# Performance work log

Measured on AMD Instinct MI355X. Metric: run time of the kernel, lower is better.

Reference implementation:

```python
import jax, jax.numpy as jnp
import numpy as np

B = 2; QD = 128; H = QD; W = QD; NQ = QD * QD
EMBED = 256; HEADS = 8; POINTS = 4; D = EMBED // HEADS; FFN = 512


def setup_inputs() -> dict:
    key = jax.random.key(0)
    ks = jax.random.split(key, 16)
    s = 0.02
    rn = lambda k, shp: jax.random.normal(k, shp, jnp.float32) * s
    return {
        'q': jax.random.normal(ks[0], (B, NQ, EMBED), jnp.float32),
        'W_off': rn(ks[1], (EMBED, HEADS * POINTS * 2)),
        'b_off': rn(ks[2], (HEADS * POINTS * 2,)),
        'W_attn': rn(ks[3], (EMBED, HEADS * POINTS)),
        'b_attn': rn(ks[4], (HEADS * POINTS,)),
        'W_val': rn(ks[5], (EMBED, EMBED)),
        'b_val': rn(ks[6], (EMBED,)),
        'W_out': rn(ks[7], (EMBED, EMBED)),
        'b_out': rn(ks[8], (EMBED,)),
        'W1': rn(ks[9], (EMBED, FFN)),
        'b1': rn(ks[10], (FFN,)),
        'W2': rn(ks[11], (FFN, EMBED)),
        'b2': rn(ks[12], (EMBED,)),
        'gamma': jnp.ones((EMBED,), jnp.float32),
        'beta': jnp.zeros((EMBED,), jnp.float32),
    }


def _layernorm(x, g, b):
    m = x.mean(-1, keepdims=True)
    v = ((x - m) ** 2).mean(-1, keepdims=True)
    return (x - m) * jax.lax.rsqrt(v + 1e-5) * g + b


def _msda(q, W_off, b_off, W_attn, b_attn, W_val, b_val, W_out, b_out):
    # value projection; value == query here. (B, NQ, EMBED)
    value = q @ W_val + b_val
    v = value.reshape(B, NQ, HEADS, D).transpose(0, 2, 1, 3)  # (B, heads, Nv, D)

    off = (q @ W_off + b_off).reshape(B, NQ, HEADS, POINTS, 2)
    aw = jax.nn.softmax((q @ W_attn + b_attn).reshape(B, NQ, HEADS, POINTS), axis=-1)

    # reference points: torch.meshgrid(linspace, linspace, indexing='xy')
    lin = jnp.linspace(0.0, 1.0, QD)
    gx, gy = jnp.meshgrid(lin, lin, indexing='xy')
    ref = jnp.stack([gx, gy], -1).reshape(1, NQ, 1, 1, 2)

    # offset_normalizer = [W, H]; sampling locations in [0,1]
    loc = ref + off / jnp.array([W, H], jnp.float32)
    # grid_sample bilinear, align_corners=False: pixel = loc * size - 0.5
    px = (loc[..., 0] * W - 0.5).transpose(0, 2, 1, 3)  # (B, heads, NQ, P)
    py = (loc[..., 1] * H - 0.5).transpose(0, 2, 1, 3)

    x0 = jnp.floor(px)
    y0 = jnp.floor(py)
    sampled = jnp.zeros((B, HEADS, NQ, POINTS, D), jnp.float32)
    for dy in (0.0, 1.0):
        for dx in (0.0, 1.0):
            xi = x0 + dx
            yi = y0 + dy
            wgt = (1.0 - jnp.abs(px - xi)) * (1.0 - jnp.abs(py - yi))
            valid = ((xi >= 0) & (xi <= W - 1) & (yi >= 0) & (yi <= H - 1)).astype(jnp.float32)
            idx = (jnp.clip(yi, 0, H - 1).astype(jnp.int32) * W
                   + jnp.clip(xi, 0, W - 1).astype(jnp.int32))  # (B, heads, NQ, P)
            g = jnp.take_along_axis(v, idx.reshape(B, HEADS, NQ * POINTS, 1), axis=2)
            g = g.reshape(B, HEADS, NQ, POINTS, D)
            sampled = sampled + g * (wgt * valid)[..., None]

    awt = aw.transpose(0, 2, 1, 3)  # (B, heads, NQ, P)
    out = (sampled * awt[..., None]).sum(3)  # (B, heads, NQ, D)
    out = out.transpose(0, 2, 1, 3).reshape(B, NQ, EMBED)
    # mmcv: dropout(output_proj(out)) + identity ; dropout is identity at eval
    return out @ W_out + b_out + q


def reference(q, W_off, b_off, W_attn, b_attn, W_val, b_val, W_out, b_out,
              W1, b1, W2, b2, gamma, beta):
    attn = _msda(q, W_off, b_off, W_attn, b_attn, W_val, b_val, W_out, b_out)
    x = attn + q  # outer residual in the module (in addition to mmcv's internal one)
    ffn = _layernorm(jax.nn.relu(x @ W1 + b1) @ W2 + b2, gamma, beta)
    return x + ffn
```

## Files before the change

kernel.cpp:

```cpp
#include <hip/hip_runtime.h>
#include <hip/hip_bf16.h>
#include <cstddef>
#include <cstdint>

#define B_      2
#define QD_     128
#define NQ_     (QD_ * QD_)
#define EMBED_  256
#define HEADS_  8
#define POINTS_ 4
#define FFN_    512
#define RTOT_   (B_ * NQ_)
#define NCATP_  384

using bf16x8 = __attribute__((ext_vector_type(8))) short;
using f32x4  = __attribute__((ext_vector_type(4))) float;

__device__ __forceinline__ short f2bf(float f) {
    unsigned u = __float_as_uint(f);
    u += 0x7FFFu + ((u >> 16) & 1u);
    return (short)(u >> 16);
}
__device__ __forceinline__ float bf2f(short s) {
    return __uint_as_float(((unsigned)(unsigned short)s) << 16);
}

#define WCAT_ELEMS  (NCATP_ * 256)
#define WOUT_ELEMS  (256 * 256)
#define W1_ELEMS    (512 * 256)
#define W2_ELEMS    (256 * 512)
#define PREP_TOTAL  (WCAT_ELEMS + WOUT_ELEMS + W1_ELEMS + W2_ELEMS)

__global__ __launch_bounds__(256) void prep_weights(
        const float* __restrict__ Wv, const float* __restrict__ Wo,
        const float* __restrict__ Wa, const float* __restrict__ bv,
        const float* __restrict__ bo, const float* __restrict__ ba,
        const float* __restrict__ W_out, const float* __restrict__ W1,
        const float* __restrict__ W2,
        short* __restrict__ WcatT, short* __restrict__ WoutT,
        short* __restrict__ W1T, short* __restrict__ W2T,
        float* __restrict__ bcat) {
    int idx = blockIdx.x * 256 + threadIdx.x;
    if (idx < WCAT_ELEMS) {
        int c = idx >> 8, k = idx & 255;
        float v = 0.f;
        if (c < 256)      v = Wv[k * 256 + c];
        else if (c < 320) v = Wo[k * 64 + (c - 256)];
        else if (c < 352) v = Wa[k * 32 + (c - 320)];
        WcatT[idx] = f2bf(v);
    } else if (idx < WCAT_ELEMS + WOUT_ELEMS) {
        int j = idx - WCAT_ELEMS; int c = j >> 8, k = j & 255;
        WoutT[j] = f2bf(W_out[k * 256 + c]);
    } else if (idx < WCAT_ELEMS + WOUT_ELEMS + W1_ELEMS) {
        int j = idx - (WCAT_ELEMS + WOUT_ELEMS); int c = j >> 8, k = j & 255;
        W1T[j] = f2bf(W1[k * 512 + c]);
    } else if (idx < PREP_TOTAL) {
        int j = idx - (WCAT_ELEMS + WOUT_ELEMS + W1_ELEMS); int c = j >> 9, k = j & 511;
        W2T[j] = f2bf(W2[k * 256 + c]);
    }
    if (idx < NCATP_) {
        float v = 0.f;
        if (idx < 256)      v = bv[idx];
        else if (idx < 320) v = bo[idx - 256];
        else if (idx < 352) v = ba[idx - 320];
        bcat[idx] = v;
    }
}

__global__ __launch_bounds__(256) void cvt_bf16(const float* __restrict__ in,
                                                short* __restrict__ out) {
    const size_t i = (size_t)blockIdx.x * 256 + threadIdx.x;
    const float4 f0 = *(const float4*)(in + i * 8);
    const float4 f1 = *(const float4*)(in + i * 8 + 4);
    bf16x8 v;
    v[0] = f2bf(f0.x); v[1] = f2bf(f0.y); v[2] = f2bf(f0.z); v[3] = f2bf(f0.w);
    v[4] = f2bf(f1.x); v[5] = f2bf(f1.y); v[6] = f2bf(f1.z); v[7] = f2bf(f1.w);
    *(bf16x8*)(out + i * 8) = v;
}

enum { EP_RELU_BF16 = 1, EP_ADD2Q_BF16 = 2, EP_SPLIT = 3 };

template <int EP>
__global__ __launch_bounds__(256) void gemm_mfma(
        const short* __restrict__ A,
        const short* __restrict__ Bt,
        const float* __restrict__ bias,
        const short* __restrict__ extra,
        float* __restrict__ Cf,
        short* __restrict__ Cb,
        int M, int N, int K) {
    __shared__ __align__(16) short As[128 * 64];
    __shared__ __align__(16) short Bs[128 * 64];

    const int t    = threadIdx.x;
    const int ln   = t & 63;
    const int w    = t >> 6;
    const int wr   = w >> 1;
    const int wc   = w & 1;
    const int lrow = ln & 15;
    const int lkg  = ln >> 4;

    const int gx   = gridDim.x;
    const int nwg  = gx * gridDim.y;
    const int flat = blockIdx.y * gx + blockIdx.x;
    const int q8   = nwg >> 3;
    const int swz  = (flat & 7) * q8 + (flat >> 3);
    const int row0 = (swz / gx) * 128;
    const int col0 = (swz % gx) * 128;

    f32x4 acc[4][4] = {};

    for (int k0 = 0; k0 < K; k0 += 64) {
        #pragma unroll
        for (int j = 0; j < 4; ++j) {
            const int c0 = (w * 4 + j) * 64;
            const int c  = c0 + ln;
            const int r  = c >> 3;
            const int s  = (c & 7) ^ (r & 7);
            const short* ga = A  + (size_t)(row0 + r) * K + (k0 + s * 8);
            const short* gb = Bt + (size_t)(col0 + r) * K + (k0 + s * 8);
            __builtin_amdgcn_global_load_lds(
                (const __attribute__((address_space(1))) void*)ga,
                (__attribute__((address_space(3))) void*)&As[c0 * 8], 16, 0, 0);
            __builtin_amdgcn_global_load_lds(
                (const __attribute__((address_space(1))) void*)gb,
                (__attribute__((address_space(3))) void*)&Bs[c0 * 8], 16, 0, 0);
        }
        __syncthreads();

        #pragma unroll
        for (int ks = 0; ks < 2; ++ks) {
            const int slot = ((ks * 4 + lkg) ^ (lrow & 7)) * 8;
            bf16x8 af[4], bfr[4];
            #pragma unroll
            for (int m = 0; m < 4; ++m)
                af[m] = *(const bf16x8*)&As[(wr * 64 + m * 16 + lrow) * 64 + slot];
            #pragma unroll
            for (int n = 0; n < 4; ++n)
                bfr[n] = *(const bf16x8*)&Bs[(wc * 64 + n * 16 + lrow) * 64 + slot];
            #pragma unroll
            for (int m = 0; m < 4; ++m)
                #pragma unroll
                for (int n = 0; n < 4; ++n)
                    acc[m][n] = __builtin_amdgcn_mfma_f32_16x16x32_bf16(
                        af[m], bfr[n], acc[m][n], 0, 0, 0);
        }
        __syncthreads();
    }

    const int orow = (ln >> 4) * 4;
    const int ocol = ln & 15;
    #pragma unroll
    for (int m = 0; m < 4; ++m) {
        #pragma unroll
        for (int n = 0; n < 4; ++n) {
            const int col = col0 + wc * 64 + n * 16 + ocol;
            const float bv = bias[col];
            #pragma unroll
            for (int rr = 0; rr < 4; ++rr) {
                const int row = row0 + wr * 64 + m * 16 + orow + rr;
                float v = acc[m][n][rr] + bv;
                if (EP == EP_SPLIT) {
                    if (col < 256) Cb[(size_t)row * 256 + col] = f2bf(v);
                    else           Cf[(size_t)row * 128 + (col - 256)] = v;
                } else if (EP == EP_RELU_BF16) {
                    Cb[(size_t)row * N + col] = f2bf(fmaxf(v, 0.f));
                } else if (EP == EP_ADD2Q_BF16) {
                    v += 2.f * bf2f(extra[(size_t)row * N + col]);
                    Cb[(size_t)row * N + col] = f2bf(v);
                }
            }
        }
    }
}

__global__ __launch_bounds__(256) void gemm_ln(
        const short* __restrict__ A,
        const short* __restrict__ Bt,
        const float* __restrict__ bias,
        const short* __restrict__ xres,
        const float* __restrict__ gamma, const float* __restrict__ beta,
        float* __restrict__ out, int M, int K) {
    __shared__ __align__(16) short As[64 * 64];
    __shared__ __align__(16) short Bs[256 * 64];
    __shared__ float red[64][4][2];

    const int t    = threadIdx.x;
    const int ln   = t & 63;
    const int w    = t >> 6;
    const int lrow = ln & 15;
    const int lkg  = ln >> 4;
    const int row0 = blockIdx.x * 64;

    f32x4 acc[4][4] = {};

    for (int k0 = 0; k0 < K; k0 += 64) {
        #pragma unroll
        for (int j = 0; j < 2; ++j) {
            const int c0 = (w * 2 + j) * 64;
            const int c  = c0 + ln;
            const int r  = c >> 3;
            const int s  = (c & 7) ^ (r & 7);
            const short* ga = A + (size_t)(row0 + r) * K + (k0 + s * 8);
            __builtin_amdgcn_global_load_lds(
                (const __attribute__((address_space(1))) void*)ga,
                (__attribute__((address_space(3))) void*)&As[c0 * 8], 16, 0, 0);
        }
        #pragma unroll
        for (int j = 0; j < 8; ++j) {
            const int c0 = (w * 8 + j) * 64;
            const int c  = c0 + ln;
            const int r  = c >> 3;
            const int s  = (c & 7) ^ (r & 7);
            const short* gb = Bt + (size_t)r * K + (k0 + s * 8);
            __builtin_amdgcn_global_load_lds(
                (const __attribute__((address_space(1))) void*)gb,
                (__attribute__((address_space(3))) void*)&Bs[c0 * 8], 16, 0, 0);
        }
        __syncthreads();

        #pragma unroll
        for (int ks = 0; ks < 2; ++ks) {
            const int slot = ((ks * 4 + lkg) ^ (lrow & 7)) * 8;
            bf16x8 af[4], bfr[4];
            #pragma unroll
            for (int m = 0; m < 4; ++m)
                af[m] = *(const bf16x8*)&As[(m * 16 + lrow) * 64 + slot];
            #pragma unroll
            for (int n = 0; n < 4; ++n)
                bfr[n] = *(const bf16x8*)&Bs[(w * 64 + n * 16 + lrow) * 64 + slot];
            #pragma unroll
            for (int m = 0; m < 4; ++m)
                #pragma unroll
                for (int n = 0; n < 4; ++n)
                    acc[m][n] = __builtin_amdgcn_mfma_f32_16x16x32_bf16(
                        af[m], bfr[n], acc[m][n], 0, 0, 0);
        }
        __syncthreads();
    }

    const int orow = (ln >> 4) * 4;
    const int ocol = ln & 15;

    #pragma unroll
    for (int n = 0; n < 4; ++n) {
        const float bv = bias[w * 64 + n * 16 + ocol];
        #pragma unroll
        for (int m = 0; m < 4; ++m)
            #pragma unroll
            for (int rr = 0; rr < 4; ++rr)
                acc[m][n][rr] += bv;
    }

    #pragma unroll
    for (int m = 0; m < 4; ++m) {
        #pragma unroll
        for (int rr = 0; rr < 4; ++rr) {
            float s = 0.f, sq = 0.f;
            #pragma unroll
            for (int n = 0; n < 4; ++n) {
                const float v = acc[m][n][rr];
                s += v; sq += v * v;
            }
            #pragma unroll
            for (int o = 1; o < 16; o <<= 1) {
                s  += __shfl_xor(s, o, 64);
                sq += __shfl_xor(sq, o, 64);
            }
            if (ocol == 0) {
                const int row = m * 16 + orow + rr;
                red[row][w][0] = s;
                red[row][w][1] = sq;
            }
        }
    }
    __syncthreads();

    #pragma unroll
    for (int m = 0; m < 4; ++m) {
        #pragma unroll
        for (int rr = 0; rr < 4; ++rr) {
            const int row = m * 16 + orow + rr;
            float S  = red[row][0][0] + red[row][1][0] + red[row][2][0] + red[row][3][0];
            float SQ = red[row][0][1] + red[row][1][1] + red[row][2][1] + red[row][3][1];
            const float mean = S * (1.0f / 256.0f);
            const float var  = SQ * (1.0f / 256.0f) - mean * mean;
            const float rs   = rsqrtf(var + 1e-5f);
            const size_t rbase = (size_t)(row0 + row) * 256;
            #pragma unroll
            for (int n = 0; n < 4; ++n) {
                const int col = w * 64 + n * 16 + ocol;
                const float o = bf2f(xres[rbase + col])
                              + (acc[m][n][rr] - mean) * rs * gamma[col] + beta[col];
                out[rbase + col] = o;
            }
        }
    }
}

__global__ __launch_bounds__(256) void msda_sample(
        const float* __restrict__ pm, const short* __restrict__ vcomp,
        short* __restrict__ msda) {
    __shared__ int   s_off[8][32][4];
    __shared__ float s_c[8][32][4];

    const int t  = threadIdx.x;
    const int r0 = blockIdx.x * 8;
    const int bq = r0 >> 14;

    {
        const int g = t >> 5, cmb = t & 31, h = cmb >> 2, p = cmb & 3;
        const int r = r0 + g;
        const int n = r & (NQ_ - 1);
        const int gi = n >> 7, gj = n & 127;
        const float* pr = pm + (size_t)r * 128;

        const float l0 = pr[64 + h * 4 + 0], l1 = pr[64 + h * 4 + 1];
        const float l2 = pr[64 + h * 4 + 2], l3 = pr[64 + h * 4 + 3];
        const float mx = fmaxf(fmaxf(l0, l1), fmaxf(l2, l3));
        const float sum = expf(l0 - mx) + expf(l1 - mx) + expf(l2 - mx) + expf(l3 - mx);
        const float lp = pr[64 + h * 4 + p];
        const float aw = expf(lp - mx) / sum;

        const float ox = pr[h * 8 + p * 2 + 0];
        const float oy = pr[h * 8 + p * 2 + 1];
        const float px = (gj * (1.0f / 127.0f) + ox * (1.0f / 128.0f)) * 128.0f - 0.5f;
        const float py = (gi * (1.0f / 127.0f) + oy * (1.0f / 128.0f)) * 128.0f - 0.5f;
        const float x0f = floorf(px), y0f = floorf(py);
        const int   x0 = (int)x0f, y0 = (int)y0f;
        const float fx = px - x0f, fy = py - y0f;
        const int x0c = min(max(x0, 0), 127), x1c = min(max(x0 + 1, 0), 127);
        const int y0c = min(max(y0, 0), 127), y1c = min(max(y0 + 1, 0), 127);
        const float vx0 = ((unsigned)x0 <= 127u) ? 1.f : 0.f;
        const float vx1 = ((unsigned)(x0 + 1) <= 127u) ? 1.f : 0.f;
        const float vy0 = ((unsigned)y0 <= 127u) ? 1.f : 0.f;
        const float vy1 = ((unsigned)(y0 + 1) <= 127u) ? 1.f : 0.f;

        s_off[g][cmb][0] = (y0c * 128 + x0c) * 512;
        s_off[g][cmb][1] = (y0c * 128 + x1c) * 512;
        s_off[g][cmb][2] = (y1c * 128 + x0c) * 512;
        s_off[g][cmb][3] = (y1c * 128 + x1c) * 512;
        s_c[g][cmb][0] = aw * (1.f - fx) * (1.f - fy) * vx0 * vy0;
        s_c[g][cmb][1] = aw * fx * (1.f - fy) * vx1 * vy0;
        s_c[g][cmb][2] = aw * (1.f - fx) * fy * vx0 * vy1;
        s_c[g][cmb][3] = aw * fx * fy * vx1 * vy1;
    }
    __syncthreads();

    const int half = t >> 7;
    const int h    = (t >> 4) & 7;
    const int dd   = t & 15;
    const char* vb = (const char*)vcomp + ((size_t)bq * NQ_ * 256 + h * 32 + dd * 2) * 2;

    #pragma unroll
    for (int it = 0; it < 4; ++it) {
        const int g = it * 2 + half;
        float a0 = 0.f, a1 = 0.f;
        #pragma unroll
        for (int p = 0; p < 4; ++p) {
            const int cmb = h * 4 + p;
            #pragma unroll
            for (int k = 0; k < 4; ++k) {
                const unsigned u = *(const unsigned*)(vb + s_off[g][cmb][k]);
                const float c = s_c[g][cmb][k];
                a0 += c * __uint_as_float(u << 16);
                a1 += c * __uint_as_float(u & 0xffff0000u);
            }
        }
        const int r = r0 + g;
        const unsigned o = (unsigned)(unsigned short)f2bf(a0)
                         | ((unsigned)(unsigned short)f2bf(a1) << 16);
        *(unsigned*)&msda[(size_t)r * 256 + h * 32 + dd * 2] = o;
    }
}

extern "C" void kernel_launch(void* const* d_in, const int* in_sizes, int n_in,
                              void* d_out, int out_size, void* d_ws, size_t ws_size,
                              hipStream_t stream) {
    const float* q      = (const float*)d_in[0];
    const float* b_out  = (const float*)d_in[8];
    const float* b1     = (const float*)d_in[10];
    const float* b2     = (const float*)d_in[12];
    const float* gamma  = (const float*)d_in[13];
    const float* beta   = (const float*)d_in[14];

    float* out = (float*)d_out;

    char* w = (char*)d_ws;
    float* pm    = (float*)w; w += (size_t)RTOT_ * 128 * 4;
    short* vcomp = (short*)w; w += (size_t)RTOT_ * 256 * 2;
    short* qbf   = (short*)w; w += (size_t)RTOT_ * EMBED_ * 2;
    short* msda  = (short*)w; w += (size_t)RTOT_ * EMBED_ * 2;
    short* xbf   = (short*)w; w += (size_t)RTOT_ * EMBED_ * 2;
    short* hid   = (short*)w; w += (size_t)RTOT_ * FFN_ * 2;
    short* WcatT = (short*)w; w += WCAT_ELEMS * 2;
    short* WoutT = (short*)w; w += WOUT_ELEMS * 2;
    short* W1T   = (short*)w; w += W1_ELEMS * 2;
    short* W2T   = (short*)w; w += W2_ELEMS * 2;
    float* bcat  = (float*)w; w += NCATP_ * 4;

    prep_weights<<<(PREP_TOTAL + 255) / 256, 256, 0, stream>>>(
        (const float*)d_in[5], (const float*)d_in[1], (const float*)d_in[3],
        (const float*)d_in[6], (const float*)d_in[2], (const float*)d_in[4],
        (const float*)d_in[7], (const float*)d_in[9], (const float*)d_in[11],
        WcatT, WoutT, W1T, W2T, bcat);

    cvt_bf16<<<(RTOT_ * EMBED_ / 8 + 255) / 256, 256, 0, stream>>>(q, qbf);

    gemm_mfma<EP_SPLIT><<<dim3(NCATP_ / 128, RTOT_ / 128), 256, 0, stream>>>(
        qbf, WcatT, bcat, nullptr, pm, vcomp, RTOT_, NCATP_, EMBED_);

    msda_sample<<<RTOT_ / 8, 256, 0, stream>>>(pm, vcomp, msda);

    gemm_mfma<EP_ADD2Q_BF16><<<dim3(EMBED_ / 128, RTOT_ / 128), 256, 0, stream>>>(
        msda, WoutT, b_out, qbf, nullptr, xbf, RTOT_, EMBED_, EMBED_);

    gemm_mfma<EP_RELU_BF16><<<dim3(FFN_ / 128, RTOT_ / 128), 256, 0, stream>>>(
        xbf, W1T, b1, nullptr, nullptr, hid, RTOT_, FFN_, EMBED_);

    gemm_ln<<<RTOT_ / 64, 256, 0, stream>>>(
        hid, W2T, b2, xbf, gamma, beta, out, RTOT_, FFN_);
}
```

Before: 107.5 us.

## Double-buffer GEMM LDS tiles, widen LN GEMM tile, merge prep kernels

Both GEMM kernels now double-buffer their LDS tiles, so the async global-to-LDS loads for the next K step are issued before the current step's MFMA work. The fused GEMM+LayerNorm kernel moves to 128-row tiles with 512 threads (8 waves), which halves how often each block reloads the full W2 tile. The q-to-bf16 conversion is merged into the weight-prep kernel to save one launch. The cost is doubled LDS use per block, which lowers occupancy, most of all for gemm_ln at about 96KB. The loop also keeps a barrier at the end of every iteration.

```diff
diff --git a/kernel.cpp b/kernel.cpp
--- a/kernel.cpp
+++ b/kernel.cpp
@@ -30,8 +30,11 @@
 #define W1_ELEMS    (512 * 256)
 #define W2_ELEMS    (256 * 512)
 #define PREP_TOTAL  (WCAT_ELEMS + WOUT_ELEMS + W1_ELEMS + W2_ELEMS)
-
-__global__ __launch_bounds__(256) void prep_weights(
+#define CVT_BLOCKS  (RTOT_ * EMBED_ / 8 / 256)
+#define PREP_BLOCKS ((PREP_TOTAL + 255) / 256)
+
+__global__ __launch_bounds__(256) void prep_all(
+        const float* __restrict__ q, short* __restrict__ qbf,
         const float* __restrict__ Wv, const float* __restrict__ Wo,
         const float* __restrict__ Wa, const float* __restrict__ bv,
         const float* __restrict__ bo, const float* __restrict__ ba,
@@ -40,7 +43,18 @@
         short* __restrict__ WcatT, short* __restrict__ WoutT,
         short* __restrict__ W1T, short* __restrict__ W2T,
         float* __restrict__ bcat) {
-    int idx = blockIdx.x * 256 + threadIdx.x;
+    const int b = blockIdx.x;
+    if (b < CVT_BLOCKS) {
+        const size_t i = (size_t)b * 256 + threadIdx.x;
+        const float4 f0 = *(const float4*)(q + i * 8);
+        const float4 f1 = *(const float4*)(q + i * 8 + 4);
+        bf16x8 v;
+        v[0] = f2bf(f0.x); v[1] = f2bf(f0.y); v[2] = f2bf(f0.z); v[3] = f2bf(f0.w);
+        v[4] = f2bf(f1.x); v[5] = f2bf(f1.y); v[6] = f2bf(f1.z); v[7] = f2bf(f1.w);
+        *(bf16x8*)(qbf + i * 8) = v;
+        return;
+    }
+    int idx = (b - CVT_BLOCKS) * 256 + threadIdx.x;
     if (idx < WCAT_ELEMS) {
         int c = idx >> 8, k = idx & 255;
         float v = 0.f;
@@ -67,17 +81,6 @@
     }
 }
 
-__global__ __launch_bounds__(256) void cvt_bf16(const float* __restrict__ in,
-                                                short* __restrict__ out) {
-    const size_t i = (size_t)blockIdx.x * 256 + threadIdx.x;
-    const float4 f0 = *(const float4*)(in + i * 8);
-    const float4 f1 = *(const float4*)(in + i * 8 + 4);
-    bf16x8 v;
-    v[0] = f2bf(f0.x); v[1] = f2bf(f0.y); v[2] = f2bf(f0.z); v[3] = f2bf(f0.w);
-    v[4] = f2bf(f1.x); v[5] = f2bf(f1.y); v[6] = f2bf(f1.z); v[7] = f2bf(f1.w);
-    *(bf16x8*)(out + i * 8) = v;
-}
-
 enum { EP_RELU_BF16 = 1, EP_ADD2Q_BF16 = 2, EP_SPLIT = 3 };
 
 template <int EP>
@@ -89,8 +92,8 @@
         float* __restrict__ Cf,
         short* __restrict__ Cb,
         int M, int N, int K) {
-    __shared__ __align__(16) short As[128 * 64];
-    __shared__ __align__(16) short Bs[128 * 64];
+    __shared__ __align__(16) short As[2][128 * 64];
+    __shared__ __align__(16) short Bs[2][128 * 64];
 
     const int t    = threadIdx.x;
     const int ln   = t & 63;
@@ -110,7 +113,7 @@
 
     f32x4 acc[4][4] = {};
 
-    for (int k0 = 0; k0 < K; k0 += 64) {
+    auto stage = [&](int buf, int k0) {
         #pragma unroll
         for (int j = 0; j < 4; ++j) {
             const int c0 = (w * 4 + j) * 64;
@@ -121,23 +124,28 @@
             const short* gb = Bt + (size_t)(col0 + r) * K + (k0 + s * 8);
             __builtin_amdgcn_global_load_lds(
                 (const __attribute__((address_space(1))) void*)ga,
-                (__attribute__((address_space(3))) void*)&As[c0 * 8], 16, 0, 0);
+                (__attribute__((address_space(3))) void*)&As[buf][c0 * 8], 16, 0, 0);
             __builtin_amdgcn_global_load_lds(
                 (const __attribute__((address_space(1))) void*)gb,
-                (__attribute__((address_space(3))) void*)&Bs[c0 * 8], 16, 0, 0);
-        }
-        __syncthreads();
-
+                (__attribute__((address_space(3))) void*)&Bs[buf][c0 * 8], 16, 0, 0);
+        }
+    };
+
+    stage(0, 0);
+    __syncthreads();
+    int cur = 0;
+    for (int k0 = 0; k0 < K; k0 += 64) {
+        if (k0 + 64 < K) stage(cur ^ 1, k0 + 64);
         #pragma unroll
         for (int ks = 0; ks < 2; ++ks) {
             const int slot = ((ks * 4 + lkg) ^ (lrow & 7)) * 8;
             bf16x8 af[4], bfr[4];
             #pragma unroll
             for (int m = 0; m < 4; ++m)
-                af[m] = *(const bf16x8*)&As[(wr * 64 + m * 16 + lrow) * 64 + slot];
+                af[m] = *(const bf16x8*)&As[cur][(wr * 64 + m * 16 + lrow) * 64 + slot];
             #pragma unroll
             for (int n = 0; n < 4; ++n)
-                bfr[n] = *(const bf16x8*)&Bs[(wc * 64 + n * 16 + lrow) * 64 + slot];
+                bfr[n] = *(const bf16x8*)&Bs[cur][(wc * 64 + n * 16 + lrow) * 64 + slot];
             #pragma unroll
             for (int m = 0; m < 4; ++m)
                 #pragma unroll
@@ -146,6 +154,7 @@
                         af[m], bfr[n], acc[m][n], 0, 0, 0);
         }
         __syncthreads();
+        cur ^= 1;
     }
 
     const int orow = (ln >> 4) * 4;
@@ -174,27 +183,29 @@
     }
 }
 
-__global__ __launch_bounds__(256) void gemm_ln(
+__global__ __launch_bounds__(512) void gemm_ln(
         const short* __restrict__ A,
         const short* __restrict__ Bt,
         const float* __restrict__ bias,
         const short* __restrict__ xres,
         const float* __restrict__ gamma, const float* __restrict__ beta,
         float* __restrict__ out, int M, int K) {
-    __shared__ __align__(16) short As[64 * 64];
-    __shared__ __align__(16) short Bs[256 * 64];
-    __shared__ float red[64][4][2];
+    __shared__ __align__(16) short As[2][128 * 64];
+    __shared__ __align__(16) short Bs[2][256 * 64];
+    __shared__ float red[128][4][2];
 
     const int t    = threadIdx.x;
     const int ln   = t & 63;
     const int w    = t >> 6;
+    const int wr   = w >> 2;
+    const int wc   = w & 3;
     const int lrow = ln & 15;
     const int lkg  = ln >> 4;
-    const int row0 = blockIdx.x * 64;
+    const int row0 = blockIdx.x * 128;
 
     f32x4 acc[4][4] = {};
 
-    for (int k0 = 0; k0 < K; k0 += 64) {
+    auto stage = [&](int buf, int k0) {
         #pragma unroll
         for (int j = 0; j < 2; ++j) {
             const int c0 = (w * 2 + j) * 64;
@@ -204,31 +215,36 @@
             const short* ga = A + (size_t)(row0 + r) * K + (k0 + s * 8);
             __builtin_amdgcn_global_load_lds(
                 (const __attribute__((address_space(1))) void*)ga,
-                (__attribute__((address_space(3))) void*)&As[c0 * 8], 16, 0, 0);
-        }
-        #pragma unroll
-        for (int j = 0; j < 8; ++j) {
-            const int c0 = (w * 8 + j) * 64;
+                (__attribute__((address_space(3))) void*)&As[buf][c0 * 8], 16, 0, 0);
+        }
+        #pragma unroll
+        for (int j = 0; j < 4; ++j) {
+            const int c0 = (w * 4 + j) * 64;
             const int c  = c0 + ln;
             const int r  = c >> 3;
             const int s  = (c & 7) ^ (r & 7);
             const short* gb = Bt + (size_t)r * K + (k0 + s * 8);
             __builtin_amdgcn_global_load_lds(
                 (const __attribute__((address_space(1))) void*)gb,
-                (__attribute__((address_space(3))) void*)&Bs[c0 * 8], 16, 0, 0);
-        }
-        __syncthreads();
-
+                (__attribute__((address_space(3))) void*)&Bs[buf][c0 * 8], 16, 0, 0);
+        }
+    };
+
+    stage(0, 0);
+    __syncthreads();
+    int cur = 0;
+    for (int k0 = 0; k0 < K; k0 += 64) {
+        if (k0 + 64 < K) stage(cur ^ 1, k0 + 64);
         #pragma unroll
         for (int ks = 0; ks < 2; ++ks) {
             const int slot = ((ks * 4 + lkg) ^ (lrow & 7)) * 8;
             bf16x8 af[4], bfr[4];
             #pragma unroll
             for (int m = 0; m < 4; ++m)
-                af[m] = *(const bf16x8*)&As[(m * 16 + lrow) * 64 + slot];
+                af[m] = *(const bf16x8*)&As[cur][(wr * 64 + m * 16 + lrow) * 64 + slot];
             #pragma unroll
             for (int n = 0; n < 4; ++n)
-                bfr[n] = *(const bf16x8*)&Bs[(w * 64 + n * 16 + lrow) * 64 + slot];
+                bfr[n] = *(const bf16x8*)&Bs[cur][(wc * 64 + n * 16 + lrow) * 64 + slot];
             #pragma unroll
             for (int m = 0; m < 4; ++m)
                 #pragma unroll
@@ -237,6 +253,7 @@
                         af[m], bfr[n], acc[m][n], 0, 0, 0);
         }
         __syncthreads();
+        cur ^= 1;
     }
 
     const int orow = (ln >> 4) * 4;
@@ -244,7 +261,7 @@
 
     #pragma unroll
     for (int n = 0; n < 4; ++n) {
-        const float bv = bias[w * 64 + n * 16 + ocol];
+        const float bv = bias[wc * 64 + n * 16 + ocol];
         #pragma unroll
         for (int m = 0; m < 4; ++m)
             #pragma unroll
@@ -268,9 +285,9 @@
                 sq += __shfl_xor(sq, o, 64);
             }
             if (ocol == 0) {
-                const int row = m * 16 + orow + rr;
-                red[row][w][0] = s;
-                red[row][w][1] = sq;
+                const int row = wr * 64 + m * 16 + orow + rr;
+                red[row][wc][0] = s;
+                red[row][wc][1] = sq;
             }
         }
     }
@@ -280,19 +297,18 @@
     for (int m = 0; m < 4; ++m) {
         #pragma unroll
         for (int rr = 0; rr < 4; ++rr) {
-            const int row = m * 16 + orow + rr;
-            float S  = red[row][0][0] + red[row][1][0] + red[row][2][0] + red[row][3][0];
-            float SQ = red[row][0][1] + red[row][1][1] + red[row][2][1] + red[row][3][1];
+            const int row = wr * 64 + m * 16 + orow + rr;
+            const float S  = red[row][0][0] + red[row][1][0] + red[row][2][0] + red[row][3][0];
+            const float SQ = red[row][0][1] + red[row][1][1] + red[row][2][1] + red[row][3][1];
             const float mean = S * (1.0f / 256.0f);
             const float var  = SQ * (1.0f / 256.0f) - mean * mean;
             const float rs   = rsqrtf(var + 1e-5f);
             const size_t rbase = (size_t)(row0 + row) * 256;
             #pragma unroll
             for (int n = 0; n < 4; ++n) {
-                const int col = w * 64 + n * 16 + ocol;
-                const float o = bf2f(xres[rbase + col])
-                              + (acc[m][n][rr] - mean) * rs * gamma[col] + beta[col];
-                out[rbase + col] = o;
+                const int col = wc * 64 + n * 16 + ocol;
+                out[rbase + col] = bf2f(xres[rbase + col])
+                                 + (acc[m][n][rr] - mean) * rs * gamma[col] + beta[col];
             }
         }
     }
@@ -399,14 +415,13 @@
     short* W2T   = (short*)w; w += W2_ELEMS * 2;
     float* bcat  = (float*)w; w += NCATP_ * 4;
 
-    prep_weights<<<(PREP_TOTAL + 255) / 256, 256, 0, stream>>>(
+    prep_all<<<CVT_BLOCKS + PREP_BLOCKS, 256, 0, stream>>>(
+        q, qbf,
         (const float*)d_in[5], (const float*)d_in[1], (const float*)d_in[3],
         (const float*)d_in[6], (const float*)d_in[2], (const float*)d_in[4],
         (const float*)d_in[7], (const float*)d_in[9], (const float*)d_in[11],
         WcatT, WoutT, W1T, W2T, bcat);
 
-    cvt_bf16<<<(RTOT_ * EMBED_ / 8 + 255) / 256, 256, 0, stream>>>(q, qbf);
-
     gemm_mfma<EP_SPLIT><<<dim3(NCATP_ / 128, RTOT_ / 128), 256, 0, stream>>>(
         qbf, WcatT, bcat, nullptr, pm, vcomp, RTOT_, NCATP_, EMBED_);
 
@@ -418,6 +433,6 @@
     gemm_mfma<EP_RELU_BF16><<<dim3(FFN_ / 128, RTOT_ / 128), 256, 0, stream>>>(
         xbf, W1T, b1, nullptr, nullptr, hid, RTOT_, FFN_, EMBED_);
 
-    gemm_ln<<<RTOT_ / 64, 256, 0, stream>>>(
+    gemm_ln<<<RTOT_ / 128, 512, 0, stream>>>(
         hid, W2T, b2, xbf, gamma, beta, out, RTOT_, FFN_);
 }
```

Result: no change. 106.7 us (-0.7%).
